# Kernel tuning notes

Hardware: AMD Instinct MI355X
Metric: run time of the kernel (lower is better)

The kernel has to match this reference:

```python
import jax, jax.numpy as jnp
import numpy as np

HEADS = 16
DIM_HEAD = 64
SCALE = DIM_HEAD ** -0.5
STEP = 0.6

def setup_inputs() -> dict:
    key = jax.random.key(0)
    ks = jax.random.split(key, 8)
    B, N, QD = 2, 2048, 1024
    M, CD = 1024, 768
    inner = HEADS * DIM_HEAD  # 1024
    return {
        "x": jax.random.normal(ks[0], (B, N, QD), jnp.float32),
        "context": jax.random.normal(ks[1], (B, M, CD), jnp.float32),
        "focused_attention_mask": jax.random.uniform(ks[2], (1, M, M), jnp.float32),
        "Wq": jax.random.normal(ks[3], (inner, QD), jnp.float32) * 0.02,
        "Wk": jax.random.normal(ks[4], (inner, CD), jnp.float32) * 0.02,
        "Wv": jax.random.normal(ks[5], (inner, CD), jnp.float32) * 0.02,
        "Wo": jax.random.normal(ks[6], (QD, inner), jnp.float32) * 0.02,
        "bo": jax.random.normal(ks[7], (QD,), jnp.float32) * 0.02,
    }

def _split_heads(t, h):
    b, n, hd = t.shape
    return t.reshape(b, n, h, hd // h).transpose(0, 2, 1, 3).reshape(b * h, n, hd // h)

def reference(x, context, focused_attention_mask, Wq, Wk, Wv, Wo, bo):
    b, n, _ = x.shape
    h = HEADS
    q = _split_heads(x @ Wq.T, h)        # (b h) n d
    k = _split_heads(context @ Wk.T, h)  # (b h) m d
    v = _split_heads(context @ Wv.T, h)
    sim = jnp.einsum('bid,bjd->bij', q, k) * SCALE  # (b h) n m
    # FCA focus-weight modulation (fam has leading dim 1, broadcast over b*h)
    fam = focused_attention_mask[0]  # (m, m)
    K = fam.shape[-1]
    fw = jnp.abs(jnp.einsum('bqk,dk->bqd', sim[:, :, :K], fam))  # (b h) n m
    fw = jnp.minimum(fw, 1.0)
    fw = fw / (jnp.max(fw, axis=2, keepdims=True) + 1e-6)
    fw = (fw > STEP).astype(sim.dtype)
    sim = sim.at[:, :, :K].add((fw - 1.0) * 50.0)
    attn = jax.nn.softmax(sim, axis=-1)
    out = jnp.einsum('bij,bjd->bid', attn, v)  # (b h) n d
    out = out.reshape(b, h, n, -1).transpose(0, 2, 1, 3).reshape(b, n, -1)
    return out @ Wo.T + bo
```

## Files before the change

### kernel.cpp

```cpp
#include <hip/hip_runtime.h>
#include <hip/hip_fp16.h>
#include <math.h>

#define SCALE 0.125f

typedef _Float16 f16;
typedef __attribute__((ext_vector_type(8))) _Float16 f16x8;
typedef __attribute__((ext_vector_type(4))) float f32x4;

#define MFMA(a, b, c) __builtin_amdgcn_mfma_f32_16x16x32_f16((a), (b), (c), 0, 0, 0)

#define LX(r, qd) (((r) << 6) + ((((qd) ^ ((r) & 7))) << 3))

__device__ __forceinline__ void gll16(const f16* g, f16* l) {
    __builtin_amdgcn_global_load_lds(
        (const __attribute__((address_space(1))) unsigned int*)(g),
        (__attribute__((address_space(3))) unsigned int*)(l),
        16, 0, 0);
}

struct SplitSeg { const float* src; f16* h; f16* l; float scale; size_t n; };
struct SplitArgs { SplitSeg seg[7]; };

__global__ __launch_bounds__(256) void split_all(SplitArgs a)
{
    SplitSeg s = a.seg[blockIdx.y];
    size_t i4 = ((size_t)blockIdx.x * 256 + threadIdx.x) * 4;
    size_t stride = (size_t)gridDim.x * 256 * 4;
    for (; i4 < s.n; i4 += stride) {
        float4 v = *(const float4*)&s.src[i4];
        float av[4] = {v.x * s.scale, v.y * s.scale, v.z * s.scale, v.w * s.scale};
        f16 hv[4], lv[4];
#pragma unroll
        for (int j = 0; j < 4; ++j) {
            hv[j] = (f16)av[j];
            lv[j] = (f16)(av[j] - (float)hv[j]);
        }
        *(float2*)&s.h[i4] = *(float2*)hv;
        *(float2*)&s.l[i4] = *(float2*)lv;
    }
}

template <int AP, int BP>
__global__ __launch_bounds__(256) void gemm16(
    const f16* __restrict__ Ah, const f16* __restrict__ Al, size_t Abat,
    const f16* __restrict__ Bh, const f16* __restrict__ Bl, int Bstr, size_t Bbat,
    float* __restrict__ Cf, const float* __restrict__ bias,
    f16* __restrict__ Ch, f16* __restrict__ Cl, int Cpitch,
    f16* __restrict__ Cth, f16* __restrict__ Ctl, int Mt,
    int Nsplit, f16* __restrict__ C2th, int Mt2,
    size_t Cbat, float oscale, int M, int N, int K)
{
    constexpr int NCH = AP * 16 + BP * 8;
    __shared__ __align__(16) f16 Ash[AP][128 * 64];
    __shared__ __align__(16) f16 Bsh[BP][64 * 64];

    const int tid  = threadIdx.x;
    const int z    = blockIdx.z;
    Ah += z * Abat; if (AP == 2) Al += z * Abat;
    Bh += z * Bbat; if (BP == 2) Bl += z * Bbat;
    const int m0   = blockIdx.y * 128;
    const int n0   = blockIdx.x * 64;
    const int w    = tid >> 6;
    const int lane = tid & 63;
    const int wm   = (w >> 1) * 64;
    const int wn   = (w & 1) * 32;
    const int lq   = lane >> 4;
    const int l15  = lane & 15;
    const int sr   = lane >> 3;
    const int sg   = lane & 7;

    f32x4 acc[4][2];
#pragma unroll
    for (int mi = 0; mi < 4; ++mi)
#pragma unroll
        for (int ni = 0; ni < 2; ++ni) acc[mi][ni] = (f32x4){0.f, 0.f, 0.f, 0.f};

    for (int k0 = 0; k0 < K; k0 += 64) {
        __syncthreads();
#pragma unroll
        for (int c = 0; c < NCH / 4; ++c) {
            int chunk = c * 4 + w;
            const f16* gp; f16* lp;
            if (chunk < AP * 16) {
                int pl = chunk >> 4, sub = chunk & 15;
                int r = sub * 8 + sr;
                int g = sg ^ (r & 7);
                gp = ((AP == 2 && pl) ? Al : Ah) + (size_t)(m0 + r) * K + k0 + g * 8;
                lp = &Ash[pl][sub * 512];
            } else {
                int cb = chunk - AP * 16;
                int pl = cb >> 3, sub = cb & 7;
                int r = sub * 8 + sr;
                int g = sg ^ (r & 7);
                gp = ((BP == 2 && pl) ? Bl : Bh) + (size_t)(n0 + r) * Bstr + k0 + g * 8;
                lp = &Bsh[pl][sub * 512];
            }
            gll16(gp, lp);
        }
        __syncthreads();

#pragma unroll
        for (int kc = 0; kc < 2; ++kc) {
            f16x8 afh[4], afl[4];
#pragma unroll
            for (int mi = 0; mi < 4; ++mi) {
                int r = wm + mi * 16 + l15;
                afh[mi] = *(const f16x8*)&Ash[0][LX(r, kc * 4 + lq)];
                if (AP == 2) afl[mi] = *(const f16x8*)&Ash[1][LX(r, kc * 4 + lq)];
            }
#pragma unroll
            for (int ni = 0; ni < 2; ++ni) {
                int r = wn + ni * 16 + l15;
                f16x8 bh = *(const f16x8*)&Bsh[0][LX(r, kc * 4 + lq)];
                f16x8 bl;
                if (BP == 2) bl = *(const f16x8*)&Bsh[1][LX(r, kc * 4 + lq)];
#pragma unroll
                for (int mi = 0; mi < 4; ++mi) {
                    f32x4 a = acc[mi][ni];
                    a = MFMA(afh[mi], bh, a);
                    if (BP == 2) a = MFMA(afh[mi], bl, a);
                    if (AP == 2) a = MFMA(afl[mi], bh, a);
                    acc[mi][ni] = a;
                }
            }
        }
    }

    const bool vhalf = (Nsplit > 0) && (n0 >= Nsplit);
    if (Cf)  Cf  += z * Cbat;
    if (Ch)  { Ch += z * Cbat; if (Cl) Cl += z * Cbat; }

#pragma unroll
    for (int mi = 0; mi < 4; ++mi) {
#pragma unroll
        for (int ni = 0; ni < 2; ++ni) {
            int row = m0 + wm + mi * 16 + lq * 4;
            int col = n0 + wn + ni * 16 + l15;
            float v[4];
#pragma unroll
            for (int r = 0; r < 4; ++r) v[r] = acc[mi][ni][r] * oscale;
            if (Cf) {
                float bb = bias ? bias[col] : 0.f;
#pragma unroll
                for (int r = 0; r < 4; ++r)
                    Cf[(size_t)(row + r) * Cpitch + col] = v[r] + bb;
            } else if (vhalf) {
                union { f16 a[4]; float2 f; } uh;
#pragma unroll
                for (int r = 0; r < 4; ++r) uh.a[r] = (f16)v[r];
                *(float2*)&C2th[(size_t)(col - Nsplit) * Mt2 + row] = uh.f;
            } else {
                if (Ch) {
#pragma unroll
                    for (int r = 0; r < 4; ++r) {
                        f16 hh = (f16)v[r];
                        Ch[(size_t)(row + r) * Cpitch + col] = hh;
                        if (Cl) Cl[(size_t)(row + r) * Cpitch + col] = (f16)(v[r] - (float)hh);
                    }
                }
                if (Cth) {
                    union { f16 a[4]; float2 f; } uh, ul;
#pragma unroll
                    for (int r = 0; r < 4; ++r) {
                        uh.a[r] = (f16)v[r];
                        ul.a[r] = (f16)(v[r] - (float)uh.a[r]);
                    }
                    *(float2*)&Cth[(size_t)col * Mt + row] = uh.f;
                    if (Ctl) *(float2*)&Ctl[(size_t)col * Mt + row] = ul.f;
                }
            }
        }
    }
}

__global__ __launch_bounds__(256) void attn_mfma(
    const f16* __restrict__ Qh, const f16* __restrict__ Ql,
    const f16* __restrict__ Kh,
    const f16* __restrict__ Gh, const f16* __restrict__ Gl,
    const f16* __restrict__ Vth, f16* __restrict__ AOh)
{
    __shared__ __align__(16) f16 Ksh[4096];
    __shared__ __align__(16) f16 Gsh[2][4096];
    __shared__ __align__(16) f16 Ps[128 * 72];
    __shared__ int eflag[4];

    const int tid = threadIdx.x;
    const int bh = blockIdx.x;
    const int b = bh >> 4, h = bh & 15;
    const int qr0 = blockIdx.y * 128;
    const int w = tid >> 6, lane = tid & 63;
    const int lq = lane >> 4, l15 = lane & 15;
    const int wq = w * 32;

    const size_t qb = ((size_t)(b * 2048 + qr0)) * 1024 + h * 64;
    const size_t kb = ((size_t)(b * 1024)) * 1024 + h * 64;
    const size_t vb = (size_t)(h * 64) * 2048 + b * 1024;

    const int sr = lane >> 3;
    const int ss = lane & 7;

    f16x8 aqh[2][2], aql[2][2];
#pragma unroll
    for (int ti = 0; ti < 2; ++ti)
#pragma unroll
        for (int kc = 0; kc < 2; ++kc) {
            size_t off = qb + (size_t)(wq + ti * 16 + l15) * 1024 + (kc * 4 + lq) * 8;
            aqh[ti][kc] = *(const f16x8*)&Qh[off];
            aql[ti][kc] = *(const f16x8*)&Ql[off];
        }

    float mx[2][4] = {};
    for (int jt = 0; jt < 16; ++jt) {
#pragma unroll
        for (int c = 0; c < 4; ++c) {
            int chunk = c * 4 + w;
            int pl = chunk >> 3, sub = chunk & 7;
            int r = sub * 8 + sr;
            int g = ss ^ (r & 7);
            const f16* gp = (pl ? Gl : Gh) + kb + (size_t)(jt * 64 + r) * 1024 + g * 8;
            gll16(gp, &Gsh[pl][sub * 512]);
        }
        __syncthreads();

#pragma unroll
        for (int tj = 0; tj < 4; ++tj) {
            f32x4 a0 = {0.f, 0.f, 0.f, 0.f}, a1 = {0.f, 0.f, 0.f, 0.f};
#pragma unroll
            for (int kc = 0; kc < 2; ++kc) {
                int lx = LX(tj * 16 + l15, kc * 4 + lq);
                f16x8 bgh = *(const f16x8*)&Gsh[0][lx];
                f16x8 bgl = *(const f16x8*)&Gsh[1][lx];
                a0 = MFMA(aqh[0][kc], bgh, a0);
                a0 = MFMA(aqh[0][kc], bgl, a0);
                a0 = MFMA(aql[0][kc], bgh, a0);
                a1 = MFMA(aqh[1][kc], bgh, a1);
                a1 = MFMA(aqh[1][kc], bgl, a1);
                a1 = MFMA(aql[1][kc], bgh, a1);
            }
#pragma unroll
            for (int r = 0; r < 4; ++r) {
                mx[0][r] = fmaxf(mx[0][r], fminf(fabsf(a0[r] * SCALE), 1.f));
                mx[1][r] = fmaxf(mx[1][r], fminf(fabsf(a1[r] * SCALE), 1.f));
            }
        }
        bool done = true;
#pragma unroll
        for (int ti = 0; ti < 2; ++ti)
#pragma unroll
            for (int r = 0; r < 4; ++r) {
                float m = mx[ti][r];
#pragma unroll
                for (int d = 1; d < 16; d <<= 1)
                    m = fmaxf(m, __shfl_xor(m, d, 64));
                mx[ti][r] = m;
                done = done && (m >= 1.0f);
            }
        int wd = __all(done ? 1 : 0);
        if (lane == 0) eflag[w] = wd;
        __syncthreads();
        if (eflag[0] && eflag[1] && eflag[2] && eflag[3]) break;
    }
    float T[2][4];
#pragma unroll
    for (int ti = 0; ti < 2; ++ti)
#pragma unroll
        for (int r = 0; r < 4; ++r)
            T[ti][r] = 4.8f * (mx[ti][r] + 1e-6f);

    const float SL2E = 0.125f * 1.44269504088896f;
    const float PEN2 = -50.0f * 1.44269504088896f;
    f32x4 aco[2][4];
#pragma unroll
    for (int ti = 0; ti < 2; ++ti)
#pragma unroll
        for (int dj = 0; dj < 4; ++dj) aco[ti][dj] = (f32x4){0.f, 0.f, 0.f, 0.f};
    float dsum[2][4] = {};

    for (int jt = 0; jt < 16; ++jt) {
        __syncthreads();
#pragma unroll
        for (int c = 0; c < 6; ++c) {
            int chunk = c * 4 + w;
            int sub = chunk & 7;
            int r = sub * 8 + sr;
            int g = ss ^ (r & 7);
            size_t off = kb + (size_t)(jt * 64 + r) * 1024 + g * 8;
            const f16* gp; f16* lp;
            if (chunk < 8)       { gp = Kh + off; lp = &Ksh[sub * 512]; }
            else if (chunk < 16) { gp = Gh + off; lp = &Gsh[0][sub * 512]; }
            else                 { gp = Gl + off; lp = &Gsh[1][sub * 512]; }
            gll16(gp, lp);
        }
        __syncthreads();

#pragma unroll
        for (int tj = 0; tj < 4; ++tj) {
            f32x4 s0 = {0.f, 0.f, 0.f, 0.f}, s1 = {0.f, 0.f, 0.f, 0.f};
            f32x4 f0 = {0.f, 0.f, 0.f, 0.f}, f1 = {0.f, 0.f, 0.f, 0.f};
#pragma unroll
            for (int kc = 0; kc < 2; ++kc) {
                int lx = LX(tj * 16 + l15, kc * 4 + lq);
                f16x8 bkh = *(const f16x8*)&Ksh[lx];
                f16x8 bgh = *(const f16x8*)&Gsh[0][lx];
                f16x8 bgl = *(const f16x8*)&Gsh[1][lx];
                s0 = MFMA(aqh[0][kc], bkh, s0);
                f0 = MFMA(aqh[0][kc], bgh, f0);
                f0 = MFMA(aqh[0][kc], bgl, f0);
                f0 = MFMA(aql[0][kc], bgh, f0);
                s1 = MFMA(aqh[1][kc], bkh, s1);
                f1 = MFMA(aqh[1][kc], bgh, f1);
                f1 = MFMA(aqh[1][kc], bgl, f1);
                f1 = MFMA(aql[1][kc], bgh, f1);
            }
#pragma unroll
            for (int r = 0; r < 4; ++r) {
                float p0 = (fabsf(f0[r]) > T[0][r]) ? 0.f : PEN2;
                f16 e0 = (f16)exp2f(fmaf(s0[r], SL2E, p0));
                Ps[(wq + lq * 4 + r) * 72 + tj * 16 + l15] = e0;
                dsum[0][r] += (float)e0;
                float p1 = (fabsf(f1[r]) > T[1][r]) ? 0.f : PEN2;
                f16 e1 = (f16)exp2f(fmaf(s1[r], SL2E, p1));
                Ps[(wq + 16 + lq * 4 + r) * 72 + tj * 16 + l15] = e1;
                dsum[1][r] += (float)e1;
            }
        }
        __syncthreads();
#pragma unroll
        for (int c = 0; c < 2; ++c) {
            int chunk = c * 4 + w;
            int sub = chunk & 7;
            int r = sub * 8 + sr;
            int g = ss ^ (r & 7);
            const f16* gp = Vth + vb + (size_t)r * 2048 + jt * 64 + g * 8;
            gll16(gp, &Ksh[sub * 512]);
        }
        __syncthreads();

#pragma unroll
        for (int kc = 0; kc < 2; ++kc) {
            f16x8 ap0 = *(const f16x8*)&Ps[(wq + l15) * 72 + kc * 32 + lq * 8];
            f16x8 ap1 = *(const f16x8*)&Ps[(wq + 16 + l15) * 72 + kc * 32 + lq * 8];
#pragma unroll
            for (int dj = 0; dj < 4; ++dj) {
                int lx = LX(dj * 16 + l15, kc * 4 + lq);
                f16x8 bvh = *(const f16x8*)&Ksh[lx];
                aco[0][dj] = MFMA(ap0, bvh, aco[0][dj]);
                aco[1][dj] = MFMA(ap1, bvh, aco[1][dj]);
            }
        }
    }

#pragma unroll
    for (int ti = 0; ti < 2; ++ti)
#pragma unroll
        for (int r = 0; r < 4; ++r) {
            float s = dsum[ti][r];
#pragma unroll
            for (int d = 1; d < 16; d <<= 1)
                s += __shfl_xor(s, d, 64);
            dsum[ti][r] = s;
        }
#pragma unroll
    for (int ti = 0; ti < 2; ++ti) {
#pragma unroll
        for (int r = 0; r < 4; ++r) {
            float invd = 1.0f / dsum[ti][r];
            int qq = qr0 + wq + ti * 16 + lq * 4 + r;
#pragma unroll
            for (int dj = 0; dj < 4; ++dj) {
                int dd = h * 64 + dj * 16 + l15;
                AOh[(size_t)(b * 2048 + qq) * 1024 + dd] = (f16)(aco[ti][dj][r] * invd);
            }
        }
    }
}

extern "C" void kernel_launch(void* const* d_in, const int* in_sizes, int n_in,
                              void* d_out, int out_size, void* d_ws, size_t ws_size,
                              hipStream_t stream)
{
    const float* x   = (const float*)d_in[0];
    const float* ctx = (const float*)d_in[1];
    const float* fam = (const float*)d_in[2];
    const float* Wq  = (const float*)d_in[3];
    const float* Wk  = (const float*)d_in[4];
    const float* Wv  = (const float*)d_in[5];
    const float* Wo  = (const float*)d_in[6];
    const float* bo  = (const float*)d_in[7];
    float* out = (float*)d_out;

    const size_t nX  = (size_t)4096 * 1024;
    const size_t nC  = (size_t)2048 * 768;
    const size_t nWq = (size_t)1024 * 1024;
    const size_t nWk = (size_t)1024 * 768;
    const size_t nF  = (size_t)1024 * 1024;
    const size_t nK  = (size_t)2048 * 1024;

    char* p = (char*)d_ws;
    f16 *xh   = (f16*)p; p += nX * 2;   f16 *xl   = (f16*)p; p += nX * 2;
    f16 *ch   = (f16*)p; p += nC * 2;   f16 *cl   = (f16*)p; p += nC * 2;
    f16 *wqh  = (f16*)p; p += nWq * 2;  f16 *wql  = (f16*)p; p += nWq * 2;
    f16 *wkvh = (f16*)p; p += nWk * 4;  f16 *wkvl = (f16*)p; p += nWk * 4;
    f16 *woh  = (f16*)p; p += nWq * 2;  f16 *wol  = (f16*)p; p += nWq * 2;
    f16 *fmh  = (f16*)p; p += nF * 2;   f16 *fml  = (f16*)p; p += nF * 2;
    f16 *qh   = (f16*)p; p += nX * 2;   f16 *ql   = (f16*)p; p += nX * 2;
    f16 *kh   = (f16*)p; p += nK * 2;
    f16 *kth  = (f16*)p; p += nK * 2;   f16 *ktl  = (f16*)p; p += nK * 2;
    f16 *vth  = (f16*)p; p += nK * 2;
    f16 *gh   = (f16*)p; p += nK * 2;   f16 *gl   = (f16*)p; p += nK * 2;
    f16 *aoh  = (f16*)p; p += nX * 2;

    const float WS  = 64.0f;
    const float IWS = 1.0f / 64.0f;

    SplitArgs sa;
    sa.seg[0] = {x,   xh,          xl,          1.f, nX};
    sa.seg[1] = {ctx, ch,          cl,          1.f, nC};
    sa.seg[2] = {Wq,  wqh,         wql,         WS,  nWq};
    sa.seg[3] = {Wk,  wkvh,        wkvl,        WS,  nWk};
    sa.seg[4] = {Wv,  wkvh + nWk,  wkvl + nWk,  WS,  nWk};
    sa.seg[5] = {Wo,  woh,         wol,         WS,  nWq};
    sa.seg[6] = {fam, fmh,         fml,         1.f, nF};
    split_all<<<dim3(64, 7), 256, 0, stream>>>(sa);

    gemm16<2, 2><<<dim3(16, 32, 1), 256, 0, stream>>>(
        xh, xl, 0, wqh, wql, 1024, 0,
        nullptr, nullptr, qh, ql, 1024, nullptr, nullptr, 0,
        0, nullptr, 0, 0, IWS, 4096, 1024, 1024);

    gemm16<2, 2><<<dim3(32, 16, 1), 256, 0, stream>>>(
        ch, cl, 0, wkvh, wkvl, 768, 0,
        nullptr, nullptr, kh, nullptr, 1024, kth, ktl, 2048,
        1024, vth, 2048, 0, IWS, 2048, 2048, 768);

    gemm16<2, 2><<<dim3(16, 8, 2), 256, 0, stream>>>(
        fmh, fml, 0, kth, ktl, 2048, 1024,
        nullptr, nullptr, gh, gl, 1024, nullptr, nullptr, 0,
        0, nullptr, 0, (size_t)1024 * 1024, 1.f, 1024, 1024, 1024);

    attn_mfma<<<dim3(32, 16), 256, 0, stream>>>(qh, ql, kh, gh, gl, vth, aoh);

    gemm16<1, 1><<<dim3(16, 32, 1), 256, 0, stream>>>(
        aoh, nullptr, 0, woh, nullptr, 1024, 0,
        out, bo, nullptr, nullptr, 1024, nullptr, nullptr, 0,
        0, nullptr, 0, 0, IWS, 4096, 1024, 1024);
}
```

Measured before the change: 295.7 us.

## Double-buffer K/G tiles and prefetch V in attention main loop

Double-buffers the K and G (high/low) shared tiles and gives V its own buffer, so the next tile's K/G loads and the current V load are issued before compute. Manual vmcnt waits and raw s_barrier replace the four __syncthreads per iteration. MFMA sections run at raised wave priority via s_setprio. This hides global-to-LDS load latency behind the MFMA work. In exchange, LDS use grows from about 42 KB to about 74 KB per block, which may reduce occupancy, and correctness now depends on the hand-counted vmcnt values.

```diff
diff --git a/kernel.cpp b/kernel.cpp
--- a/kernel.cpp
+++ b/kernel.cpp
@@ -180,8 +180,9 @@
     const f16* __restrict__ Gh, const f16* __restrict__ Gl,
     const f16* __restrict__ Vth, f16* __restrict__ AOh)
 {
-    __shared__ __align__(16) f16 Ksh[4096];
-    __shared__ __align__(16) f16 Gsh[2][4096];
+    __shared__ __align__(16) f16 Ksh[2][4096];
+    __shared__ __align__(16) f16 Gsh[2][2][4096];
+    __shared__ __align__(16) f16 Vsh[4096];
     __shared__ __align__(16) f16 Ps[128 * 72];
     __shared__ int eflag[4];
 
@@ -219,7 +220,7 @@
             int r = sub * 8 + sr;
             int g = ss ^ (r & 7);
             const f16* gp = (pl ? Gl : Gh) + kb + (size_t)(jt * 64 + r) * 1024 + g * 8;
-            gll16(gp, &Gsh[pl][sub * 512]);
+            gll16(gp, &Gsh[0][pl][sub * 512]);
         }
         __syncthreads();
 
@@ -229,8 +230,8 @@
 #pragma unroll
             for (int kc = 0; kc < 2; ++kc) {
                 int lx = LX(tj * 16 + l15, kc * 4 + lq);
-                f16x8 bgh = *(const f16x8*)&Gsh[0][lx];
-                f16x8 bgl = *(const f16x8*)&Gsh[1][lx];
+                f16x8 bgh = *(const f16x8*)&Gsh[0][0][lx];
+                f16x8 bgl = *(const f16x8*)&Gsh[0][1][lx];
                 a0 = MFMA(aqh[0][kc], bgh, a0);
                 a0 = MFMA(aqh[0][kc], bgl, a0);
                 a0 = MFMA(aql[0][kc], bgh, a0);
@@ -277,33 +278,64 @@
         for (int dj = 0; dj < 4; ++dj) aco[ti][dj] = (f32x4){0.f, 0.f, 0.f, 0.f};
     float dsum[2][4] = {};
 
+#pragma unroll
+    for (int c = 0; c < 6; ++c) {
+        int chunk = c * 4 + w;
+        int sub = chunk & 7;
+        int r = sub * 8 + sr;
+        int g = ss ^ (r & 7);
+        size_t off = kb + (size_t)r * 1024 + g * 8;
+        const f16* gp; f16* lp;
+        if (chunk < 8)       { gp = Kh + off; lp = &Ksh[0][sub * 512]; }
+        else if (chunk < 16) { gp = Gh + off; lp = &Gsh[0][0][sub * 512]; }
+        else                 { gp = Gl + off; lp = &Gsh[0][1][sub * 512]; }
+        gll16(gp, lp);
+    }
+
     for (int jt = 0; jt < 16; ++jt) {
-        __syncthreads();
-#pragma unroll
-        for (int c = 0; c < 6; ++c) {
+        const int cur = jt & 1;
+
+#pragma unroll
+        for (int c = 0; c < 2; ++c) {
             int chunk = c * 4 + w;
             int sub = chunk & 7;
             int r = sub * 8 + sr;
             int g = ss ^ (r & 7);
-            size_t off = kb + (size_t)(jt * 64 + r) * 1024 + g * 8;
-            const f16* gp; f16* lp;
-            if (chunk < 8)       { gp = Kh + off; lp = &Ksh[sub * 512]; }
-            else if (chunk < 16) { gp = Gh + off; lp = &Gsh[0][sub * 512]; }
-            else                 { gp = Gl + off; lp = &Gsh[1][sub * 512]; }
-            gll16(gp, lp);
-        }
-        __syncthreads();
+            const f16* gp = Vth + vb + (size_t)r * 2048 + jt * 64 + g * 8;
+            gll16(gp, &Vsh[sub * 512]);
+        }
+        if (jt < 15) {
+#pragma unroll
+            for (int c = 0; c < 6; ++c) {
+                int chunk = c * 4 + w;
+                int sub = chunk & 7;
+                int r = sub * 8 + sr;
+                int g = ss ^ (r & 7);
+                size_t off = kb + (size_t)((jt + 1) * 64 + r) * 1024 + g * 8;
+                const f16* gp; f16* lp;
+                if (chunk < 8)       { gp = Kh + off; lp = &Ksh[cur ^ 1][sub * 512]; }
+                else if (chunk < 16) { gp = Gh + off; lp = &Gsh[cur ^ 1][0][sub * 512]; }
+                else                 { gp = Gl + off; lp = &Gsh[cur ^ 1][1][sub * 512]; }
+                gll16(gp, lp);
+            }
+            asm volatile("s_waitcnt vmcnt(8)" ::: "memory");
+        } else {
+            asm volatile("s_waitcnt vmcnt(2)" ::: "memory");
+        }
+        __builtin_amdgcn_s_barrier();
+        __builtin_amdgcn_sched_barrier(0);
 
 #pragma unroll
         for (int tj = 0; tj < 4; ++tj) {
             f32x4 s0 = {0.f, 0.f, 0.f, 0.f}, s1 = {0.f, 0.f, 0.f, 0.f};
             f32x4 f0 = {0.f, 0.f, 0.f, 0.f}, f1 = {0.f, 0.f, 0.f, 0.f};
+            __builtin_amdgcn_s_setprio(1);
 #pragma unroll
             for (int kc = 0; kc < 2; ++kc) {
                 int lx = LX(tj * 16 + l15, kc * 4 + lq);
-                f16x8 bkh = *(const f16x8*)&Ksh[lx];
-                f16x8 bgh = *(const f16x8*)&Gsh[0][lx];
-                f16x8 bgl = *(const f16x8*)&Gsh[1][lx];
+                f16x8 bkh = *(const f16x8*)&Ksh[cur][lx];
+                f16x8 bgh = *(const f16x8*)&Gsh[cur][0][lx];
+                f16x8 bgl = *(const f16x8*)&Gsh[cur][1][lx];
                 s0 = MFMA(aqh[0][kc], bkh, s0);
                 f0 = MFMA(aqh[0][kc], bgh, f0);
                 f0 = MFMA(aqh[0][kc], bgl, f0);
@@ -313,6 +345,7 @@
                 f1 = MFMA(aqh[1][kc], bgl, f1);
                 f1 = MFMA(aql[1][kc], bgh, f1);
             }
+            __builtin_amdgcn_s_setprio(0);
 #pragma unroll
             for (int r = 0; r < 4; ++r) {
                 float p0 = (fabsf(f0[r]) > T[0][r]) ? 0.f : PEN2;
@@ -325,18 +358,15 @@
                 dsum[1][r] += (float)e1;
             }
         }
-        __syncthreads();
-#pragma unroll
-        for (int c = 0; c < 2; ++c) {
-            int chunk = c * 4 + w;
-            int sub = chunk & 7;
-            int r = sub * 8 + sr;
-            int g = ss ^ (r & 7);
-            const f16* gp = Vth + vb + (size_t)r * 2048 + jt * 64 + g * 8;
-            gll16(gp, &Ksh[sub * 512]);
-        }
-        __syncthreads();
-
+
+        if (jt < 15) asm volatile("s_waitcnt vmcnt(6)" ::: "memory");
+        else         asm volatile("s_waitcnt vmcnt(0)" ::: "memory");
+        asm volatile("s_waitcnt lgkmcnt(0)" ::: "memory");
+        __builtin_amdgcn_sched_barrier(0);
+        __builtin_amdgcn_s_barrier();
+        __builtin_amdgcn_sched_barrier(0);
+
+        __builtin_amdgcn_s_setprio(1);
 #pragma unroll
         for (int kc = 0; kc < 2; ++kc) {
             f16x8 ap0 = *(const f16x8*)&Ps[(wq + l15) * 72 + kc * 32 + lq * 8];
@@ -344,11 +374,17 @@
 #pragma unroll
             for (int dj = 0; dj < 4; ++dj) {
                 int lx = LX(dj * 16 + l15, kc * 4 + lq);
-                f16x8 bvh = *(const f16x8*)&Ksh[lx];
+                f16x8 bvh = *(const f16x8*)&Vsh[lx];
                 aco[0][dj] = MFMA(ap0, bvh, aco[0][dj]);
                 aco[1][dj] = MFMA(ap1, bvh, aco[1][dj]);
             }
         }
+        __builtin_amdgcn_s_setprio(0);
+
+        asm volatile("s_waitcnt lgkmcnt(0)" ::: "memory");
+        __builtin_amdgcn_sched_barrier(0);
+        __builtin_amdgcn_s_barrier();
+        __builtin_amdgcn_sched_barrier(0);
     }
 
 #pragma unroll
```

Measured after the change: 278.9 us. 1.06x faster.
